# Kernel tuning notes

Hardware: AMD Instinct MI355X
Metric: run time of the kernel (lower is better)

Reference implementation:

```python
import jax, jax.numpy as jnp
import numpy as np

B, N, H = 128, 2048, 128
FEAT = 15


def setup_inputs() -> dict:
    key = jax.random.key(0)
    ks = jax.random.split(key, 24)
    f32 = jnp.float32
    inp = {
        'x':   jax.random.normal(ks[0], (B, N), f32),
        'x1':  jax.random.uniform(ks[1], (B, N), f32),
        'x2':  jax.random.uniform(ks[2], (B, N), f32),
        'z1':  jax.random.uniform(ks[3], (B, N), f32),
        'z2':  jax.random.uniform(ks[4], (B, N), f32),
        'x1E': jax.random.uniform(ks[5], (B, N), f32),
        'x2E': jax.random.uniform(ks[6], (B, N), f32),
        'z1E': jax.random.uniform(ks[7], (B, N), f32),
        'z2E': jax.random.uniform(ks[8], (B, N), f32),
        'muB': jax.random.uniform(ks[9], (B, 1), f32, 0.01, 0.1),
        'lb':  jax.random.normal(ks[10], (B, N), f32) - 2.0,
        'ub':  jax.random.normal(ks[11], (B, N), f32) + 2.0,
        'has_lb': jnp.ones((B, N), bool),
        'has_ub': jnp.ones((B, N), bool),
        # LSTM params (PyTorch gate order i, f, g, o)
        'W_ih': 0.1 * jax.random.normal(ks[12], (4 * H, FEAT), f32),
        'W_hh': 0.1 * jax.random.normal(ks[13], (4 * H, H), f32),
        'b_ih': 0.1 * jax.random.normal(ks[14], (4 * H,), f32),
        'b_hh': 0.1 * jax.random.normal(ks[15], (4 * H,), f32),
        # px_head: Linear(H,H) -> ReLU -> Linear(H,1)
        'W1': 0.1 * jax.random.normal(ks[16], (H, H), f32),
        'b1': 0.1 * jax.random.normal(ks[17], (H,), f32),
        'W2': 0.1 * jax.random.normal(ks[18], (1, H), f32),
        'b2': 0.1 * jax.random.normal(ks[19], (1,), f32),
    }
    return inp


def _forward(x, x1, x2, z1, z2, x1E, x2E, z1E, z2E, muB, lb, ub,
             W_ih, W_hh, b_ih, b_hh, W1, b1, W2, b2, has_lb, has_ub):
    Bb, n = x.shape
    eps = 1e-12
    # slack / bad-coordinate handling
    z1 = jnp.where((z1 + muB) <= 0, 0.0, z1)
    z2 = jnp.where((z2 + muB) <= 0, 0.0, z2)
    # quadratic merit stand-in: M = 0.5(||x||^2 + ||z1||^2 + ||z2||^2)
    grad_x, grad_z1, grad_z2 = x, z1, z2
    invD1 = jnp.clip((z1 + muB) / (x1 + muB + eps), 0.0, 100.0)
    invD2 = jnp.clip((z2 + muB) / (x2 + muB + eps), 0.0, 100.0)
    muB_bn = jnp.broadcast_to(muB, (Bb, n))
    # [B, n, 15] -> [B*n, 15]
    feat = jnp.stack([x, x1, x2, z1, z2, grad_x, grad_z1, grad_z2,
                      x1E, x2E, z1E, z2E, muB_bn, invD1, invD2], axis=-1)
    feat = feat.reshape(Bb * n, FEAT)
    # single-step LSTM cell, h0 = c0 = 0 so W_hh @ h0 vanishes
    gates = feat @ W_ih.T + b_ih + b_hh          # [B*n, 4H]
    i, f, g, o = jnp.split(gates, 4, axis=-1)
    c = jax.nn.sigmoid(i) * jnp.tanh(g)
    h = jax.nn.sigmoid(o) * jnp.tanh(c)          # [B*n, H]
    # MLP head -> per-coordinate positive step size
    p = jax.nn.relu(h @ W1.T + b1) @ W2.T + b2   # [B*n, 1]
    p_x = jnp.abs(p).reshape(Bb, n)
    # elementwise updates
    d_x = -p_x * grad_x
    x_new = x + d_x
    z1 = z1 - invD1 * (-p_x * grad_x + grad_z1)
    z2 = z2 - invD2 * (p_x * grad_x + grad_z2)
    x = x_new  # project_step = identity accept
    x1 = jnp.where(has_lb, x - lb, 0.0)
    x2 = jnp.where(has_ub, ub - x, 0.0)
    return jnp.concatenate([x, x1, x2, z1, z2], axis=-1)  # [B, 5n]


def reference(x, x1, x2, z1, z2, x1E, x2E, z1E, z2E, muB, lb, ub,
              has_lb, has_ub, W_ih, W_hh, b_ih, b_hh, W1, b1, W2, b2):
    return _forward(x, x1, x2, z1, z2, x1E, x2E, z1E, z2E, muB, lb, ub,
                    W_ih, W_hh, b_ih, b_hh, W1, b1, W2, b2, has_lb, has_ub)
```

## Files before the change

### kernel.cpp

```cpp
#include <hip/hip_runtime.h>


typedef _Float16 half8v  __attribute__((ext_vector_type(8)));
typedef _Float16 half4v  __attribute__((ext_vector_type(4)));
typedef float    float4v __attribute__((ext_vector_type(4)));

#define N_SZ   2048
#define ROWS   262144
#define BLOCKT 512
#define NWAVES 8
#define NBLK   1024
#define WROWS  32

__device__ __forceinline__ float fast_rcp(float x) { return __builtin_amdgcn_rcpf(x); }
__device__ __forceinline__ float sigm(float x)  { return fast_rcp(1.0f + __expf(-x)); }
__device__ __forceinline__ float tanh_f(float x){ return 1.0f - 2.0f * fast_rcp(1.0f + __expf(2.0f * x)); }
__device__ __forceinline__ float tanh_c(float y) {
    const float t = y * y;
    return y * __builtin_fmaf(t, __builtin_fmaf(t, __builtin_fmaf(t,
            -0.02714f, 0.12052f), -0.33157f), 0.99986f);
}

__global__ __launch_bounds__(BLOCKT)
void ps_lstm_k16b(const float* __restrict__ x_,
                  const float* __restrict__ x1_,
                  const float* __restrict__ x2_,
                  const float* __restrict__ z1_,
                  const float* __restrict__ z2_,
                  const float* __restrict__ x1E_,
                  const float* __restrict__ x2E_,
                  const float* __restrict__ z1E_,
                  const float* __restrict__ z2E_,
                  const float* __restrict__ muB_,
                  const float* __restrict__ lb_,
                  const float* __restrict__ ub_,
                  const float* __restrict__ Wih_,
                  const float* __restrict__ bih_,
                  const float* __restrict__ bhh_,
                  const float* __restrict__ W1_,
                  const float* __restrict__ b1_,
                  const float* __restrict__ W2_,
                  const float* __restrict__ b2_,
                  float* __restrict__ out_)
{
    __shared__ __align__(16) _Float16 fragWih[3 * 8 * 64 * 4];
    __shared__ __align__(16) _Float16 fragW1 [8 * 8 * 64 * 4];
    __shared__ __align__(16) _Float16 sFeat[NWAVES][WROWS * 16];

    const int tid  = threadIdx.x;
    const int lane = tid & 63;
    const int w    = tid >> 6;
    const int c    = lane & 15;
    const int q    = lane >> 4;

    for (int ch = tid; ch < 3 * 8 * 64; ch += BLOCKT) {
        const int g   = ch >> 9;
        const int rem = ch & 511;
        const int kk  = rem >> 6;
        const int l   = rem & 63;
        const int m   = kk * 16 + (l & 15);
        const int q4  = l >> 4;
        const int grow = (g == 0 ? m : (g == 1 ? 256 + m : 384 + m));
        half4v hh;
        #pragma unroll
        for (int j = 0; j < 4; ++j) {
            const int k = q4 * 4 + j;
            const float v = (k < 15) ? Wih_[grow * 15 + k]
                                     : (bih_[grow] + bhh_[grow]);
            hh[j] = (_Float16)v;
        }
        *(half4v*)&fragWih[(size_t)ch * 4] = hh;
    }
    for (int ch = tid; ch < 8 * 8 * 64; ch += BLOCKT) {
        const int nt = ch >> 9;
        const int kk = (ch >> 6) & 7;
        const int l  = ch & 63;
        const int n2 = nt * 16 + (l & 15);
        const int k0 = kk * 16 + (l >> 4) * 4;
        const float4 a = *(const float4*)&W1_[n2 * 128 + k0];
        half4v hh;
        hh[0] = (_Float16)a.x; hh[1] = (_Float16)a.y;
        hh[2] = (_Float16)a.z; hh[3] = (_Float16)a.w;
        *(half4v*)&fragW1[(size_t)ch * 4] = hh;
    }

    float b1r[8], w2r[8];
    #pragma unroll
    for (int nt = 0; nt < 8; ++nt) {
        b1r[nt] = b1_[nt * 16 + c];
        w2r[nt] = W2_[nt * 16 + c];
    }
    const float b2v = b2_[0];

    __syncthreads();

    const int rbase = (blockIdx.x * NWAVES + w) * WROWS;

    float ex = 0.f, ez1 = 0.f, ez2 = 0.f, eD1 = 0.f, eD2 = 0.f, elb = 0.f, eub = 0.f;
    if (lane < WROWS) {
        const int r = rbase + lane;
        const float x   = x_[r];
        const float x1  = x1_[r];
        const float x2  = x2_[r];
        float       z1  = z1_[r];
        float       z2  = z2_[r];
        const float x1E = x1E_[r];
        const float x2E = x2E_[r];
        const float z1E = z1E_[r];
        const float z2E = z2E_[r];
        const float mu  = muB_[r >> 11];

        z1 = ((z1 + mu) <= 0.0f) ? 0.0f : z1;
        z2 = ((z2 + mu) <= 0.0f) ? 0.0f : z2;
        float invD1 = (z1 + mu) * fast_rcp(x1 + mu + 1e-12f);
        float invD2 = (z2 + mu) * fast_rcp(x2 + mu + 1e-12f);
        invD1 = fminf(fmaxf(invD1, 0.0f), 100.0f);
        invD2 = fminf(fmaxf(invD2, 0.0f), 100.0f);

        const float f[15] = { x, x1, x2, z1, z2, x, z1, z2,
                              x1E, x2E, z1E, z2E, mu, invD1, invD2 };
        half8v f0, f1;
        #pragma unroll
        for (int k = 0; k < 8; ++k) f0[k] = (_Float16)f[k];
        #pragma unroll
        for (int k = 0; k < 7; ++k) f1[k] = (_Float16)f[8 + k];
        f1[7] = (_Float16)1.0f;
        *(half8v*)&sFeat[w][lane * 16]     = f0;
        *(half8v*)&sFeat[w][lane * 16 + 8] = f1;

        ex = x; ez1 = z1; ez2 = z2; eD1 = invD1; eD2 = invD2;
        elb = lb_[r]; eub = ub_[r];
    }

    float pr0 = 0.f, pr1 = 0.f;

    #pragma unroll 1
    for (int rh = 0; rh < 2; ++rh) {
        const half4v fB = *(const half4v*)&sFeat[w][(rh * 16 + c) * 16 + q * 4];

        float4v acc0 = {0.f,0.f,0.f,0.f}, acc1 = {0.f,0.f,0.f,0.f};
        float4v acc2 = {0.f,0.f,0.f,0.f}, acc3 = {0.f,0.f,0.f,0.f};
        float4v acc4 = {0.f,0.f,0.f,0.f}, acc5 = {0.f,0.f,0.f,0.f};
        float4v acc6 = {0.f,0.f,0.f,0.f}, acc7 = {0.f,0.f,0.f,0.f};

        #pragma unroll 1
        for (int kk = 0; kk < 8; ++kk) {
            const half4v Ai = *(const half4v*)&fragWih[((0 * 8 + kk) * 64 + lane) * 4];
            const half4v Ag = *(const half4v*)&fragWih[((1 * 8 + kk) * 64 + lane) * 4];
            const half4v Ao = *(const half4v*)&fragWih[((2 * 8 + kk) * 64 + lane) * 4];
            const float4v zc = {0.f, 0.f, 0.f, 0.f};
            float4v di = __builtin_amdgcn_mfma_f32_16x16x16f16(Ai, fB, zc, 0, 0, 0);
            float4v dg = __builtin_amdgcn_mfma_f32_16x16x16f16(Ag, fB, zc, 0, 0, 0);
            float4v dv = __builtin_amdgcn_mfma_f32_16x16x16f16(Ao, fB, zc, 0, 0, 0);
            half4v hB;
            #pragma unroll
            for (int j = 0; j < 4; ++j) {
                const float cv = sigm(di[j]) * tanh_f(dg[j]);
                hB[j] = (_Float16)(sigm(dv[j]) * tanh_c(cv));
            }
#define HSTEP(NT, ACC) { \
            const half4v Bw = *(const half4v*)&fragW1[(((NT) * 8 + kk) * 64 + lane) * 4]; \
            ACC = __builtin_amdgcn_mfma_f32_16x16x16f16(hB, Bw, ACC, 0, 0, 0); }
            HSTEP(0, acc0)  HSTEP(1, acc1)
            HSTEP(2, acc2)  HSTEP(3, acc3)
            HSTEP(4, acc4)  HSTEP(5, acc5)
            HSTEP(6, acc6)  HSTEP(7, acc7)
#undef HSTEP
        }

        float p0 = 0.f, p1 = 0.f, p2 = 0.f, p3 = 0.f;
#define EPI(NT, ACC) { \
        const float bb = b1r[NT], ww = w2r[NT]; \
        p0 = __builtin_fmaf(fmaxf(ACC[0] + bb, 0.f), ww, p0); \
        p1 = __builtin_fmaf(fmaxf(ACC[1] + bb, 0.f), ww, p1); \
        p2 = __builtin_fmaf(fmaxf(ACC[2] + bb, 0.f), ww, p2); \
        p3 = __builtin_fmaf(fmaxf(ACC[3] + bb, 0.f), ww, p3); }
        EPI(0, acc0)  EPI(1, acc1)  EPI(2, acc2)  EPI(3, acc3)
        EPI(4, acc4)  EPI(5, acc5)  EPI(6, acc6)  EPI(7, acc7)
#undef EPI
        #pragma unroll
        for (int s = 1; s <= 8; s <<= 1) {
            p0 += __shfl_xor(p0, s, 64);
            p1 += __shfl_xor(p1, s, 64);
            p2 += __shfl_xor(p2, s, 64);
            p3 += __shfl_xor(p3, s, 64);
        }
        const int srcl = ((lane >> 2) & 3) * 16;
        const float s0v = __shfl(p0, srcl, 64);
        const float s1v = __shfl(p1, srcl, 64);
        const float s2v = __shfl(p2, srcl, 64);
        const float s3v = __shfl(p3, srcl, 64);
        const float sA  = (lane & 1) ? s1v : s0v;
        const float sB  = (lane & 1) ? s3v : s2v;
        const float ps  = (lane & 2) ? sB : sA;
        if (rh == 0) pr0 = ps; else pr1 = ps;
    }

    if (lane < WROWS) {
        const int   r     = rbase + lane;
        const int   b     = r >> 11;
        const int   n     = r & (N_SZ - 1);
        const float p     = ((lane < 16) ? pr0 : pr1) + b2v;
        const float pxx   = fabsf(p) * ex;
        const float x_new = ex - pxx;
        float* ob = out_ + (size_t)b * (5 * N_SZ) + n;
        ob[0 * N_SZ] = x_new;
        ob[1 * N_SZ] = x_new - elb;
        ob[2 * N_SZ] = eub - x_new;
        ob[3 * N_SZ] = ez1 - eD1 * (ez1 - pxx);
        ob[4 * N_SZ] = ez2 - eD2 * (ez2 + pxx);
    }
}

extern "C" void kernel_launch(void* const* d_in, const int* in_sizes, int n_in,
                              void* d_out, int out_size, void* d_ws, size_t ws_size,
                              hipStream_t stream) {
    (void)in_sizes; (void)n_in; (void)out_size; (void)d_ws; (void)ws_size;
    const float* x_   = (const float*)d_in[0];
    const float* x1_  = (const float*)d_in[1];
    const float* x2_  = (const float*)d_in[2];
    const float* z1_  = (const float*)d_in[3];
    const float* z2_  = (const float*)d_in[4];
    const float* x1E_ = (const float*)d_in[5];
    const float* x2E_ = (const float*)d_in[6];
    const float* z1E_ = (const float*)d_in[7];
    const float* z2E_ = (const float*)d_in[8];
    const float* muB_ = (const float*)d_in[9];
    const float* lb_  = (const float*)d_in[10];
    const float* ub_  = (const float*)d_in[11];
    const float* Wih_ = (const float*)d_in[14];
    const float* bih_ = (const float*)d_in[16];
    const float* bhh_ = (const float*)d_in[17];
    const float* W1_  = (const float*)d_in[18];
    const float* b1_  = (const float*)d_in[19];
    const float* W2_  = (const float*)d_in[20];
    const float* b2_  = (const float*)d_in[21];
    float* out_ = (float*)d_out;

    ps_lstm_k16b<<<NBLK, BLOCKT, 0, stream>>>(
        x_, x1_, x2_, z1_, z2_, x1E_, x2E_, z1E_, z2E_, muB_, lb_, ub_,
        Wih_, bih_, bhh_, W1_, b1_, W2_, b2_, out_);
}
```

Measured before the change: 141.7 us.

## Split gate and head MFMA phases, fuse activations, reuse weights across two tiles

Each wave now handles two 32-row tiles in a loop and the grid is halved, so the shared-memory weight fragment setup is amortised over twice as much work. Inside each 16-row half the kernel first computes all eight gate MFMA groups and their activations into eight register fragments, then runs the 64 head MFMAs back to back. This separates the dependent MFMA-then-activation chains from the accumulation chain. The sigmoid times tanh product is folded into one expression with a single reciprocal to cut transcendental and rcp count. The costs are higher register pressure from the eight live hB fragments and fewer blocks available to hide latency.

```diff
diff --git a/kernel.cpp b/kernel.cpp
--- a/kernel.cpp
+++ b/kernel.cpp
@@ -9,39 +9,35 @@
 #define ROWS   262144
 #define BLOCKT 512
 #define NWAVES 8
-#define NBLK   1024
+#define NBLK   512
+#define WITERS 2
 #define WROWS  32
 
 __device__ __forceinline__ float fast_rcp(float x) { return __builtin_amdgcn_rcpf(x); }
-__device__ __forceinline__ float sigm(float x)  { return fast_rcp(1.0f + __expf(-x)); }
-__device__ __forceinline__ float tanh_f(float x){ return 1.0f - 2.0f * fast_rcp(1.0f + __expf(2.0f * x)); }
 __device__ __forceinline__ float tanh_c(float y) {
     const float t = y * y;
     return y * __builtin_fmaf(t, __builtin_fmaf(t, __builtin_fmaf(t,
             -0.02714f, 0.12052f), -0.33157f), 0.99986f);
 }
+__device__ __forceinline__ float act_h(float i, float g, float o) {
+    const float u  = __expf(-i);
+    const float vv = __expf(2.0f * fminf(g, 40.0f));
+    const float cv = (vv - 1.0f) * fast_rcp((1.0f + u) * (1.0f + vv));
+    const float ho = fast_rcp(1.0f + __expf(-o));
+    return ho * tanh_c(cv);
+}
 
 __global__ __launch_bounds__(BLOCKT)
-void ps_lstm_k16b(const float* __restrict__ x_,
-                  const float* __restrict__ x1_,
-                  const float* __restrict__ x2_,
-                  const float* __restrict__ z1_,
-                  const float* __restrict__ z2_,
-                  const float* __restrict__ x1E_,
-                  const float* __restrict__ x2E_,
-                  const float* __restrict__ z1E_,
-                  const float* __restrict__ z2E_,
-                  const float* __restrict__ muB_,
-                  const float* __restrict__ lb_,
-                  const float* __restrict__ ub_,
-                  const float* __restrict__ Wih_,
-                  const float* __restrict__ bih_,
-                  const float* __restrict__ bhh_,
-                  const float* __restrict__ W1_,
-                  const float* __restrict__ b1_,
-                  const float* __restrict__ W2_,
-                  const float* __restrict__ b2_,
-                  float* __restrict__ out_)
+void ps_lstm_ph(const float* __restrict__ x_,  const float* __restrict__ x1_,
+                const float* __restrict__ x2_, const float* __restrict__ z1_,
+                const float* __restrict__ z2_, const float* __restrict__ x1E_,
+                const float* __restrict__ x2E_,const float* __restrict__ z1E_,
+                const float* __restrict__ z2E_,const float* __restrict__ muB_,
+                const float* __restrict__ lb_, const float* __restrict__ ub_,
+                const float* __restrict__ Wih_,const float* __restrict__ bih_,
+                const float* __restrict__ bhh_,const float* __restrict__ W1_,
+                const float* __restrict__ b1_, const float* __restrict__ W2_,
+                const float* __restrict__ b2_, float* __restrict__ out_)
 {
     __shared__ __align__(16) _Float16 fragWih[3 * 8 * 64 * 4];
     __shared__ __align__(16) _Float16 fragW1 [8 * 8 * 64 * 4];
@@ -83,7 +79,6 @@
         hh[2] = (_Float16)a.z; hh[3] = (_Float16)a.w;
         *(half4v*)&fragW1[(size_t)ch * 4] = hh;
     }
-
     float b1r[8], w2r[8];
     #pragma unroll
     for (int nt = 0; nt < 8; ++nt) {
@@ -94,121 +89,127 @@
 
     __syncthreads();
 
-    const int rbase = (blockIdx.x * NWAVES + w) * WROWS;
-
-    float ex = 0.f, ez1 = 0.f, ez2 = 0.f, eD1 = 0.f, eD2 = 0.f, elb = 0.f, eub = 0.f;
-    if (lane < WROWS) {
-        const int r = rbase + lane;
-        const float x   = x_[r];
-        const float x1  = x1_[r];
-        const float x2  = x2_[r];
-        float       z1  = z1_[r];
-        float       z2  = z2_[r];
-        const float x1E = x1E_[r];
-        const float x2E = x2E_[r];
-        const float z1E = z1E_[r];
-        const float z2E = z2E_[r];
-        const float mu  = muB_[r >> 11];
-
-        z1 = ((z1 + mu) <= 0.0f) ? 0.0f : z1;
-        z2 = ((z2 + mu) <= 0.0f) ? 0.0f : z2;
-        float invD1 = (z1 + mu) * fast_rcp(x1 + mu + 1e-12f);
-        float invD2 = (z2 + mu) * fast_rcp(x2 + mu + 1e-12f);
-        invD1 = fminf(fmaxf(invD1, 0.0f), 100.0f);
-        invD2 = fminf(fmaxf(invD2, 0.0f), 100.0f);
-
-        const float f[15] = { x, x1, x2, z1, z2, x, z1, z2,
-                              x1E, x2E, z1E, z2E, mu, invD1, invD2 };
-        half8v f0, f1;
-        #pragma unroll
-        for (int k = 0; k < 8; ++k) f0[k] = (_Float16)f[k];
-        #pragma unroll
-        for (int k = 0; k < 7; ++k) f1[k] = (_Float16)f[8 + k];
-        f1[7] = (_Float16)1.0f;
-        *(half8v*)&sFeat[w][lane * 16]     = f0;
-        *(half8v*)&sFeat[w][lane * 16 + 8] = f1;
-
-        ex = x; ez1 = z1; ez2 = z2; eD1 = invD1; eD2 = invD2;
-        elb = lb_[r]; eub = ub_[r];
-    }
-
-    float pr0 = 0.f, pr1 = 0.f;
-
     #pragma unroll 1
-    for (int rh = 0; rh < 2; ++rh) {
-        const half4v fB = *(const half4v*)&sFeat[w][(rh * 16 + c) * 16 + q * 4];
-
-        float4v acc0 = {0.f,0.f,0.f,0.f}, acc1 = {0.f,0.f,0.f,0.f};
-        float4v acc2 = {0.f,0.f,0.f,0.f}, acc3 = {0.f,0.f,0.f,0.f};
-        float4v acc4 = {0.f,0.f,0.f,0.f}, acc5 = {0.f,0.f,0.f,0.f};
-        float4v acc6 = {0.f,0.f,0.f,0.f}, acc7 = {0.f,0.f,0.f,0.f};
+    for (int it = 0; it < WITERS; ++it) {
+        const int rbase = (((int)blockIdx.x * NWAVES + w) * WITERS + it) * WROWS;
+
+        float ex = 0.f, ez1 = 0.f, ez2 = 0.f, eD1 = 0.f, eD2 = 0.f, elb = 0.f, eub = 0.f;
+        if (lane < WROWS) {
+            const int r = rbase + lane;
+            const float x   = x_[r];
+            const float x1  = x1_[r];
+            const float x2  = x2_[r];
+            float       z1  = z1_[r];
+            float       z2  = z2_[r];
+            const float mu  = muB_[r >> 11];
+            z1 = ((z1 + mu) <= 0.0f) ? 0.0f : z1;
+            z2 = ((z2 + mu) <= 0.0f) ? 0.0f : z2;
+            float invD1 = (z1 + mu) * fast_rcp(x1 + mu + 1e-12f);
+            float invD2 = (z2 + mu) * fast_rcp(x2 + mu + 1e-12f);
+            invD1 = fminf(fmaxf(invD1, 0.0f), 100.0f);
+            invD2 = fminf(fmaxf(invD2, 0.0f), 100.0f);
+            const float f[15] = { x, x1, x2, z1, z2, x, z1, z2,
+                                  x1E_[r], x2E_[r], z1E_[r], z2E_[r], mu, invD1, invD2 };
+            half8v f0, f1;
+            #pragma unroll
+            for (int k = 0; k < 8; ++k) f0[k] = (_Float16)f[k];
+            #pragma unroll
+            for (int k = 0; k < 7; ++k) f1[k] = (_Float16)f[8 + k];
+            f1[7] = (_Float16)1.0f;
+            *(half8v*)&sFeat[w][lane * 16]     = f0;
+            *(half8v*)&sFeat[w][lane * 16 + 8] = f1;
+            ex = x; ez1 = z1; ez2 = z2; eD1 = invD1; eD2 = invD2;
+            elb = lb_[r]; eub = ub_[r];
+        }
+
+        float pr0 = 0.f, pr1 = 0.f;
 
         #pragma unroll 1
-        for (int kk = 0; kk < 8; ++kk) {
-            const half4v Ai = *(const half4v*)&fragWih[((0 * 8 + kk) * 64 + lane) * 4];
-            const half4v Ag = *(const half4v*)&fragWih[((1 * 8 + kk) * 64 + lane) * 4];
-            const half4v Ao = *(const half4v*)&fragWih[((2 * 8 + kk) * 64 + lane) * 4];
-            const float4v zc = {0.f, 0.f, 0.f, 0.f};
-            float4v di = __builtin_amdgcn_mfma_f32_16x16x16f16(Ai, fB, zc, 0, 0, 0);
-            float4v dg = __builtin_amdgcn_mfma_f32_16x16x16f16(Ag, fB, zc, 0, 0, 0);
-            float4v dv = __builtin_amdgcn_mfma_f32_16x16x16f16(Ao, fB, zc, 0, 0, 0);
-            half4v hB;
+        for (int rh = 0; rh < 2; ++rh) {
+            const half4v fB = *(const half4v*)&sFeat[w][(rh * 16 + c) * 16 + q * 4];
+
+            half4v hB0, hB1, hB2, hB3, hB4, hB5, hB6, hB7;
+#define GSTEP(KK, HB) { \
+            const half4v Ai = *(const half4v*)&fragWih[((0 * 8 + (KK)) * 64 + lane) * 4]; \
+            const half4v Ag = *(const half4v*)&fragWih[((1 * 8 + (KK)) * 64 + lane) * 4]; \
+            const half4v Ao = *(const half4v*)&fragWih[((2 * 8 + (KK)) * 64 + lane) * 4]; \
+            const float4v zc = {0.f, 0.f, 0.f, 0.f}; \
+            const float4v di = __builtin_amdgcn_mfma_f32_16x16x16f16(Ai, fB, zc, 0, 0, 0); \
+            const float4v dg = __builtin_amdgcn_mfma_f32_16x16x16f16(Ag, fB, zc, 0, 0, 0); \
+            const float4v dv = __builtin_amdgcn_mfma_f32_16x16x16f16(Ao, fB, zc, 0, 0, 0); \
+            HB[0] = (_Float16)act_h(di[0], dg[0], dv[0]); \
+            HB[1] = (_Float16)act_h(di[1], dg[1], dv[1]); \
+            HB[2] = (_Float16)act_h(di[2], dg[2], dv[2]); \
+            HB[3] = (_Float16)act_h(di[3], dg[3], dv[3]); }
+            GSTEP(0, hB0)  GSTEP(1, hB1)  GSTEP(2, hB2)  GSTEP(3, hB3)
+            GSTEP(4, hB4)  GSTEP(5, hB5)  GSTEP(6, hB6)  GSTEP(7, hB7)
+#undef GSTEP
+
+            float4v acc0 = {0,0,0,0}, acc1 = {0,0,0,0}, acc2 = {0,0,0,0}, acc3 = {0,0,0,0};
+            float4v acc4 = {0,0,0,0}, acc5 = {0,0,0,0}, acc6 = {0,0,0,0}, acc7 = {0,0,0,0};
+#define HKK(KK, HB) { \
+            const half4v B0 = *(const half4v*)&fragW1[((0 * 8 + (KK)) * 64 + lane) * 4]; \
+            acc0 = __builtin_amdgcn_mfma_f32_16x16x16f16(HB, B0, acc0, 0, 0, 0); \
+            const half4v B1 = *(const half4v*)&fragW1[((1 * 8 + (KK)) * 64 + lane) * 4]; \
+            acc1 = __builtin_amdgcn_mfma_f32_16x16x16f16(HB, B1, acc1, 0, 0, 0); \
+            const half4v B2 = *(const half4v*)&fragW1[((2 * 8 + (KK)) * 64 + lane) * 4]; \
+            acc2 = __builtin_amdgcn_mfma_f32_16x16x16f16(HB, B2, acc2, 0, 0, 0); \
+            const half4v B3 = *(const half4v*)&fragW1[((3 * 8 + (KK)) * 64 + lane) * 4]; \
+            acc3 = __builtin_amdgcn_mfma_f32_16x16x16f16(HB, B3, acc3, 0, 0, 0); \
+            const half4v B4 = *(const half4v*)&fragW1[((4 * 8 + (KK)) * 64 + lane) * 4]; \
+            acc4 = __builtin_amdgcn_mfma_f32_16x16x16f16(HB, B4, acc4, 0, 0, 0); \
+            const half4v B5 = *(const half4v*)&fragW1[((5 * 8 + (KK)) * 64 + lane) * 4]; \
+            acc5 = __builtin_amdgcn_mfma_f32_16x16x16f16(HB, B5, acc5, 0, 0, 0); \
+            const half4v B6 = *(const half4v*)&fragW1[((6 * 8 + (KK)) * 64 + lane) * 4]; \
+            acc6 = __builtin_amdgcn_mfma_f32_16x16x16f16(HB, B6, acc6, 0, 0, 0); \
+            const half4v B7 = *(const half4v*)&fragW1[((7 * 8 + (KK)) * 64 + lane) * 4]; \
+            acc7 = __builtin_amdgcn_mfma_f32_16x16x16f16(HB, B7, acc7, 0, 0, 0); }
+            HKK(0, hB0)  HKK(1, hB1)  HKK(2, hB2)  HKK(3, hB3)
+            HKK(4, hB4)  HKK(5, hB5)  HKK(6, hB6)  HKK(7, hB7)
+#undef HKK
+
+            float p0 = 0.f, p1 = 0.f, p2 = 0.f, p3 = 0.f;
+#define EPI(NT, ACC) { \
+            const float bb = b1r[NT], ww = w2r[NT]; \
+            p0 = __builtin_fmaf(fmaxf(ACC[0] + bb, 0.f), ww, p0); \
+            p1 = __builtin_fmaf(fmaxf(ACC[1] + bb, 0.f), ww, p1); \
+            p2 = __builtin_fmaf(fmaxf(ACC[2] + bb, 0.f), ww, p2); \
+            p3 = __builtin_fmaf(fmaxf(ACC[3] + bb, 0.f), ww, p3); }
+            EPI(0, acc0)  EPI(1, acc1)  EPI(2, acc2)  EPI(3, acc3)
+            EPI(4, acc4)  EPI(5, acc5)  EPI(6, acc6)  EPI(7, acc7)
+#undef EPI
             #pragma unroll
-            for (int j = 0; j < 4; ++j) {
-                const float cv = sigm(di[j]) * tanh_f(dg[j]);
-                hB[j] = (_Float16)(sigm(dv[j]) * tanh_c(cv));
+            for (int s = 1; s <= 8; s <<= 1) {
+                p0 += __shfl_xor(p0, s, 64);
+                p1 += __shfl_xor(p1, s, 64);
+                p2 += __shfl_xor(p2, s, 64);
+                p3 += __shfl_xor(p3, s, 64);
             }
-#define HSTEP(NT, ACC) { \
-            const half4v Bw = *(const half4v*)&fragW1[(((NT) * 8 + kk) * 64 + lane) * 4]; \
-            ACC = __builtin_amdgcn_mfma_f32_16x16x16f16(hB, Bw, ACC, 0, 0, 0); }
-            HSTEP(0, acc0)  HSTEP(1, acc1)
-            HSTEP(2, acc2)  HSTEP(3, acc3)
-            HSTEP(4, acc4)  HSTEP(5, acc5)
-            HSTEP(6, acc6)  HSTEP(7, acc7)
-#undef HSTEP
-        }
-
-        float p0 = 0.f, p1 = 0.f, p2 = 0.f, p3 = 0.f;
-#define EPI(NT, ACC) { \
-        const float bb = b1r[NT], ww = w2r[NT]; \
-        p0 = __builtin_fmaf(fmaxf(ACC[0] + bb, 0.f), ww, p0); \
-        p1 = __builtin_fmaf(fmaxf(ACC[1] + bb, 0.f), ww, p1); \
-        p2 = __builtin_fmaf(fmaxf(ACC[2] + bb, 0.f), ww, p2); \
-        p3 = __builtin_fmaf(fmaxf(ACC[3] + bb, 0.f), ww, p3); }
-        EPI(0, acc0)  EPI(1, acc1)  EPI(2, acc2)  EPI(3, acc3)
-        EPI(4, acc4)  EPI(5, acc5)  EPI(6, acc6)  EPI(7, acc7)
-#undef EPI
-        #pragma unroll
-        for (int s = 1; s <= 8; s <<= 1) {
-            p0 += __shfl_xor(p0, s, 64);
-            p1 += __shfl_xor(p1, s, 64);
-            p2 += __shfl_xor(p2, s, 64);
-            p3 += __shfl_xor(p3, s, 64);
-        }
-        const int srcl = ((lane >> 2) & 3) * 16;
-        const float s0v = __shfl(p0, srcl, 64);
-        const float s1v = __shfl(p1, srcl, 64);
-        const float s2v = __shfl(p2, srcl, 64);
-        const float s3v = __shfl(p3, srcl, 64);
-        const float sA  = (lane & 1) ? s1v : s0v;
-        const float sB  = (lane & 1) ? s3v : s2v;
-        const float ps  = (lane & 2) ? sB : sA;
-        if (rh == 0) pr0 = ps; else pr1 = ps;
-    }
-
-    if (lane < WROWS) {
-        const int   r     = rbase + lane;
-        const int   b     = r >> 11;
-        const int   n     = r & (N_SZ - 1);
-        const float p     = ((lane < 16) ? pr0 : pr1) + b2v;
-        const float pxx   = fabsf(p) * ex;
-        const float x_new = ex - pxx;
-        float* ob = out_ + (size_t)b * (5 * N_SZ) + n;
-        ob[0 * N_SZ] = x_new;
-        ob[1 * N_SZ] = x_new - elb;
-        ob[2 * N_SZ] = eub - x_new;
-        ob[3 * N_SZ] = ez1 - eD1 * (ez1 - pxx);
-        ob[4 * N_SZ] = ez2 - eD2 * (ez2 + pxx);
+            const int srcl = ((lane >> 2) & 3) * 16;
+            const float s0v = __shfl(p0, srcl, 64);
+            const float s1v = __shfl(p1, srcl, 64);
+            const float s2v = __shfl(p2, srcl, 64);
+            const float s3v = __shfl(p3, srcl, 64);
+            const float sA  = (lane & 1) ? s1v : s0v;
+            const float sB  = (lane & 1) ? s3v : s2v;
+            const float ps  = (lane & 2) ? sB : sA;
+            if (rh == 0) pr0 = ps; else pr1 = ps;
+        }
+
+        if (lane < WROWS) {
+            const int   r     = rbase + lane;
+            const int   b     = r >> 11;
+            const int   n     = r & (N_SZ - 1);
+            const float p     = ((lane < 16) ? pr0 : pr1) + b2v;
+            const float pxx   = fabsf(p) * ex;
+            const float x_new = ex - pxx;
+            float* ob = out_ + (size_t)b * (5 * N_SZ) + n;
+            ob[0 * N_SZ] = x_new;
+            ob[1 * N_SZ] = x_new - elb;
+            ob[2 * N_SZ] = eub - x_new;
+            ob[3 * N_SZ] = ez1 - eD1 * (ez1 - pxx);
+            ob[4 * N_SZ] = ez2 - eD2 * (ez2 + pxx);
+        }
     }
 }
 
@@ -237,7 +238,7 @@
     const float* b2_  = (const float*)d_in[21];
     float* out_ = (float*)d_out;
 
-    ps_lstm_k16b<<<NBLK, BLOCKT, 0, stream>>>(
+    ps_lstm_ph<<<NBLK, BLOCKT, 0, stream>>>(
         x_, x1_, x2_, z1_, z2_, x1E_, x2E_, z1E_, z2E_, muB_, lb_, ub_,
         Wih_, bih_, bhh_, W1_, b1_, W2_, b2_, out_);
 }
```

Measured after the change: 154.8 us. 9.2% more time.
